# Kernel optimization log

Hardware: AMD Instinct MI355X
Metric: run time of the kernel (lower is better)

## Reference

```python
import jax, jax.numpy as jnp
import numpy as np

# Production-scale dims: batch, feature dim, number of hierarchy classes.
B, F, C = 4096, 1024, 2047
DEPTH = 11  # perfect binary tree: levels 0..10, C = 2**11 - 1, parent(i) = (i-1)//2

# Static per-level node index arrays (numpy, so the jitted code sees constants).
LEVELS = [np.arange(2 ** l - 1, 2 ** (l + 1) - 1) for l in range(DEPTH)]


def setup_inputs() -> dict:
    key = jax.random.key(0)
    k1, k2, k3 = jax.random.split(key, 3)
    x = jax.random.normal(k1, (B, F), jnp.float32)
    weight = jax.random.normal(k2, (C, F), jnp.float32) * 0.02  # nn.Linear weight (C, F)
    bias = jnp.zeros((C,), jnp.float32)
    # Original zero-inits pairs; we use small random values so the CRF is non-trivial.
    pairs = jax.random.normal(k3, (C, C, 2, 2), jnp.float32) * 0.1
    return {"x": x, "weight": weight, "bias": bias, "pairs": pairs}


def _crf_marginals(emissions, pairs):
    """Tree-CRF sum-product (forward/backward style) over a binary label tree.

    emissions: (B, C, 2) log-potentials per node per binary label.
    pairs: (C, C, 2, 2); pairs[i, j, yi, yj] is the edge potential for parent i,
    child j (only tree edges are consumed, matching TreeCRFLayer).
    Returns per-node marginal probabilities (B, C, 2).
    """
    alphas = jnp.zeros_like(emissions)
    # Upward messages: leaves -> root, one vectorized step per tree level.
    for l in range(DEPTH - 1, 0, -1):
        idx = LEVELS[l]
        par = (idx - 1) // 2
        local = emissions[:, idx] + alphas[:, idx]                    # (B, n, 2) child label
        pe = pairs[par, idx]                                          # (n, 2, 2) [y_par, y_child]
        msg = jax.nn.logsumexp(pe[None] + local[:, :, None, :], axis=3)  # (B, n, 2)
        alphas = alphas.at[:, par].add(msg)  # siblings share a parent -> scatter-add
    betas = jnp.zeros_like(emissions)
    # Downward messages: root -> leaves.
    for l in range(DEPTH - 1):
        idx = LEVELS[l]
        local = emissions[:, idx] + betas[:, idx]                     # (B, n, 2) parent label
        for ch in (2 * idx + 1, 2 * idx + 2):
            pe = pairs[idx, ch]                                       # (n, 2, 2)
            msg = jax.nn.logsumexp(local[:, :, :, None] + pe[None], axis=2)  # (B, n, 2)
            betas = betas.at[:, ch].set(msg)  # exactly one parent per node
    scores = emissions + alphas + betas
    return jax.nn.softmax(scores, axis=2)  # normalize per node over the 2 labels


def reference(x, weight, bias, pairs):
    e = x @ weight.T + bias                   # (B, C) = Linear(n_features -> n_classes)
    emissions = jnp.stack((-e, e), axis=2)    # (B, C, 2)
    return _crf_marginals(emissions, pairs)[:, :, 1]
```

## Files before the change

kernel.cpp:

```cpp
#include <hip/hip_runtime.h>
#include <math.h>

#define B_DIM 4096
#define F_DIM 1024
#define C_DIM 2047
#define C_PAD 2048
#define DEPTH 11

#define LOG2E 1.4426950408889634f

typedef __attribute__((ext_vector_type(8))) short bf16x8;
typedef __attribute__((ext_vector_type(4))) float f32x4;

#define AS1(p) ((const __attribute__((address_space(1))) void*)(p))
#define AS3(p) ((__attribute__((address_space(3))) void*)(p))

__device__ __forceinline__ unsigned short f2bf(float f) {
    unsigned int u = __float_as_uint(f);
    unsigned int r = (u + 0x7fffu + ((u >> 16) & 1u)) >> 16;
    return (unsigned short)r;
}

#define XTOT (B_DIM * F_DIM)
#define WTOT (C_PAD * F_DIM)

__global__ __launch_bounds__(256) void cvt_kernel(
    const float* __restrict__ x, const float* __restrict__ w,
    unsigned short* __restrict__ xb, unsigned short* __restrict__ wb)
{
    const int i = (blockIdx.x * 256 + threadIdx.x) * 4;
    if (i < XTOT) {
        float4 v = *(const float4*)(x + i);
        ushort4 h;
        h.x = f2bf(v.x); h.y = f2bf(v.y); h.z = f2bf(v.z); h.w = f2bf(v.w);
        *(ushort4*)(xb + i) = h;
    } else {
        const int j = i - XTOT;
        const int row = j >> 10;
        ushort4 h = {0, 0, 0, 0};
        if (row < C_DIM) {
            float4 v = *(const float4*)(w + j);
            h.x = f2bf(v.x); h.y = f2bf(v.y); h.z = f2bf(v.z); h.w = f2bf(v.w);
        }
        *(ushort4*)(wb + j) = h;
    }
}

__global__ __launch_bounds__(256) void pack_kernel(
    const float* __restrict__ pairs, float* __restrict__ pk)
{
    const int c = blockIdx.x * 256 + threadIdx.x;
    if (c >= 1 && c < C_DIM) {
        const int p = (c - 1) >> 1;
        float4 v = *(const float4*)(pairs + ((size_t)p * C_DIM + c) * 4);
        pk[c + 1]        = v.x * LOG2E;
        pk[c + 1 + 2048] = v.y * LOG2E;
        pk[c + 1 + 4096] = v.z * LOG2E;
        pk[c + 1 + 6144] = v.w * LOG2E;
    }
}

__global__ __launch_bounds__(256) void gemm_bf16_kernel(
    const unsigned short* __restrict__ xb, const unsigned short* __restrict__ wb,
    const float* __restrict__ bias, float* __restrict__ eb)
{
    __shared__ unsigned short smemA[128 * 32];
    __shared__ unsigned short smemB[128 * 32];

    const int tid  = threadIdx.x;
    const int lane = tid & 63;
    const int wave = tid >> 6;
    const int wr = wave >> 1, wc = wave & 1;

    const int lin = blockIdx.x + blockIdx.y * gridDim.x;
    const int wg  = (lin & 7) * 64 + (lin >> 3);
    const int bn = wg & 15, bm = wg >> 4;

    f32x4 acc[4][4] = {};
    const int r0 = tid >> 2,         c0 = tid & 3;
    const int r1 = (tid + 256) >> 2, c1 = tid & 3;
    const int sc0 = ((c0 ^ ((r0 >> 1) & 3)) << 3);
    const int sc1 = ((c1 ^ ((r1 >> 1) & 3)) << 3);

    const size_t arow0 = (size_t)(bm * 128 + r0) * F_DIM;
    const size_t arow1 = (size_t)(bm * 128 + r1) * F_DIM;
    const size_t brow0 = (size_t)(bn * 128 + r0) * F_DIM;
    const size_t brow1 = (size_t)(bn * 128 + r1) * F_DIM;

    unsigned short* ldsA0 = smemA + wave * 512;
    unsigned short* ldsA1 = smemA + 2048 + wave * 512;
    unsigned short* ldsB0 = smemB + wave * 512;
    unsigned short* ldsB1 = smemB + 2048 + wave * 512;

    const int fra = wr * 64 + (lane & 15);
    const int frb = wc * 64 + (lane & 15);
    const int kc  = lane >> 4;

    for (int k0 = 0; k0 < F_DIM; k0 += 32) {
        __builtin_amdgcn_global_load_lds(AS1(xb + arow0 + k0 + sc0), AS3(ldsA0), 16, 0, 0);
        __builtin_amdgcn_global_load_lds(AS1(xb + arow1 + k0 + sc1), AS3(ldsA1), 16, 0, 0);
        __builtin_amdgcn_global_load_lds(AS1(wb + brow0 + k0 + sc0), AS3(ldsB0), 16, 0, 0);
        __builtin_amdgcn_global_load_lds(AS1(wb + brow1 + k0 + sc1), AS3(ldsB1), 16, 0, 0);
        __syncthreads();

        bf16x8 af[4], bfr[4];
#pragma unroll
        for (int m = 0; m < 4; ++m) {
            const int row = fra + m * 16;
            af[m] = *(const bf16x8*)(smemA + row * 32 + ((kc ^ ((row >> 1) & 3)) << 3));
        }
#pragma unroll
        for (int n = 0; n < 4; ++n) {
            const int row = frb + n * 16;
            bfr[n] = *(const bf16x8*)(smemB + row * 32 + ((kc ^ ((row >> 1) & 3)) << 3));
        }
#pragma unroll
        for (int m = 0; m < 4; ++m)
#pragma unroll
            for (int n = 0; n < 4; ++n)
                acc[m][n] = __builtin_amdgcn_mfma_f32_16x16x32_bf16(
                    af[m], bfr[n], acc[m][n], 0, 0, 0);
        __syncthreads();
    }

    const int colbase = bn * 128 + wc * 64 + (lane & 15);
    const int rowbase = bm * 128 + wr * 64 + ((lane >> 4) << 2);
#pragma unroll
    for (int m = 0; m < 4; ++m)
#pragma unroll
        for (int n = 0; n < 4; ++n) {
            const int gc = colbase + n * 16;
            if (gc < C_DIM) {
                const float bv = bias[gc];
#pragma unroll
                for (int r = 0; r < 4; ++r)
                    eb[(size_t)(rowbase + m * 16 + r) * C_PAD + gc + 1] = acc[m][n][r] + bv;
            }
        }
}

#define BMF 64
#define BNF 64
#define BKF 16

__global__ __launch_bounds__(256) void gemm_f32_kernel(
    const float* __restrict__ x, const float* __restrict__ w,
    const float* __restrict__ bias, float* __restrict__ e)
{
    __shared__ float As[BKF][BMF];
    __shared__ float Bs[BKF][BNF];
    const int bn = blockIdx.x, bm = blockIdx.y;
    const int tid = threadIdx.x;
    const int tx = tid & 15, ty = tid >> 4;
    const int m0 = ty * 4, n0 = tx * 4;
    const int lrow = tid >> 2, lc4 = (tid & 3) * 4;
    const int gm = bm * BMF + lrow;
    const int gn = bn * BNF + lrow;
    const bool wvalid = (gn < C_DIM);
    const float* xp = x + (size_t)gm * F_DIM + lc4;
    const float* wp = wvalid ? (w + (size_t)gn * F_DIM + lc4) : w;
    float acc[4][4] = {};
    for (int k0 = 0; k0 < F_DIM; k0 += BKF) {
        float4 av = *(const float4*)(xp + k0);
        float4 bv = make_float4(0.f, 0.f, 0.f, 0.f);
        if (wvalid) bv = *(const float4*)(wp + k0);
        As[lc4 + 0][lrow] = av.x; As[lc4 + 1][lrow] = av.y;
        As[lc4 + 2][lrow] = av.z; As[lc4 + 3][lrow] = av.w;
        Bs[lc4 + 0][lrow] = bv.x; Bs[lc4 + 1][lrow] = bv.y;
        Bs[lc4 + 2][lrow] = bv.z; Bs[lc4 + 3][lrow] = bv.w;
        __syncthreads();
#pragma unroll
        for (int k = 0; k < BKF; ++k) {
            float4 a = *(const float4*)&As[k][m0];
            float4 b = *(const float4*)&Bs[k][n0];
            acc[0][0] += a.x * b.x; acc[0][1] += a.x * b.y; acc[0][2] += a.x * b.z; acc[0][3] += a.x * b.w;
            acc[1][0] += a.y * b.x; acc[1][1] += a.y * b.y; acc[1][2] += a.y * b.z; acc[1][3] += a.y * b.w;
            acc[2][0] += a.z * b.x; acc[2][1] += a.z * b.y; acc[2][2] += a.z * b.z; acc[2][3] += a.z * b.w;
            acc[3][0] += a.w * b.x; acc[3][1] += a.w * b.y; acc[3][2] += a.w * b.z; acc[3][3] += a.w * b.w;
        }
        __syncthreads();
    }
    const int gmo = bm * BMF + m0, gno = bn * BNF + n0;
#pragma unroll
    for (int i = 0; i < 4; ++i)
#pragma unroll
        for (int j = 0; j < 4; ++j) {
            int n = gno + j;
            if (n < C_DIM) e[(size_t)(gmo + i) * C_DIM + n] = acc[i][j] + bias[n];
        }
}

__device__ __forceinline__ float lse2_2(float a, float b) {
    float m = fmaxf(a, b);
    return m + __log2f(1.f + exp2f(fminf(a, b) - m));
}
__device__ __forceinline__ float sigmoid2(float d) {
    return __builtin_amdgcn_rcpf(1.f + exp2f(-d));
}

__global__ __launch_bounds__(256) void crf_wave_kernel(
    const float* __restrict__ pk,
    const float* __restrict__ eb,
    float* __restrict__ out)
{
    const int lane = threadIdx.x & 63;
    const int row  = blockIdx.x * 4 + (threadIdx.x >> 6);
    const float* ebr = eb + (size_t)row * C_PAD;
    float* orow = out + (size_t)row * C_DIM;
    const float* pkx = pk;
    const float* pky = pk + 2048;
    const float* pkz = pk + 4096;
    const float* pkw = pk + 6144;

    float el[4][4];
    float da9[4][2];
#pragma unroll
    for (int q = 0; q < 4; ++q) {
        const int bi = 1024 + 4 * lane + 256 * q;
        float4 ev = *(const float4*)(ebr + bi);
        float4 k4x = *(const float4*)(pkx + bi);
        float4 k4y = *(const float4*)(pky + bi);
        float4 k4z = *(const float4*)(pkz + bi);
        float4 k4w = *(const float4*)(pkw + bi);
        float er[4] = {ev.x * LOG2E, ev.y * LOG2E, ev.z * LOG2E, ev.w * LOG2E};
        float xr[4] = {k4x.x, k4x.y, k4x.z, k4x.w};
        float yr[4] = {k4y.x, k4y.y, k4y.z, k4y.w};
        float zr[4] = {k4z.x, k4z.y, k4z.z, k4z.w};
        float wr4[4] = {k4w.x, k4w.y, k4w.z, k4w.w};
        float dm[4];
#pragma unroll
        for (int r = 0; r < 4; ++r) {
            el[q][r] = er[r];
            dm[r] = lse2_2(zr[r] - er[r], wr4[r] + er[r])
                  - lse2_2(xr[r] - er[r], yr[r] + er[r]);
        }
        da9[q][0] = dm[0] + dm[1];
        da9[q][1] = dm[2] + dm[3];
    }

    float e9[4][2], da8[4];
#pragma unroll
    for (int q = 0; q < 4; ++q) {
        const int bi = 512 + 2 * lane + 128 * q;
        float2 ev = *(const float2*)(ebr + bi);
        float2 k2x = *(const float2*)(pkx + bi);
        float2 k2y = *(const float2*)(pky + bi);
        float2 k2z = *(const float2*)(pkz + bi);
        float2 k2w = *(const float2*)(pkw + bi);
        e9[q][0] = ev.x * LOG2E; e9[q][1] = ev.y * LOG2E;
        float dm0 = lse2_2(k2z.x - e9[q][0], k2w.x + e9[q][0] + da9[q][0])
                  - lse2_2(k2x.x - e9[q][0], k2y.x + e9[q][0] + da9[q][0]);
        float dm1 = lse2_2(k2z.y - e9[q][1], k2w.y + e9[q][1] + da9[q][1])
                  - lse2_2(k2x.y - e9[q][1], k2y.y + e9[q][1] + da9[q][1]);
        da8[q] = dm0 + dm1;
    }

    float e8[4], ps8[4];
#pragma unroll
    for (int q = 0; q < 4; ++q) {
        const int bi = 256 + lane + 64 * q;
        e8[q] = ebr[bi] * LOG2E;
        float kx = pkx[bi], ky = pky[bi], kz = pkz[bi], kw = pkw[bi];
        float dm = lse2_2(kz - e8[q], kw + e8[q] + da8[q])
                 - lse2_2(kx - e8[q], ky + e8[q] + da8[q]);
        ps8[q] = dm + __shfl_xor(dm, 1, 64);
    }
    float da7[2];
    {
        const int s = (2 * lane) & 63;
        float t00 = __shfl(ps8[0], s, 64), t01 = __shfl(ps8[1], s, 64);
        float t10 = __shfl(ps8[2], s, 64), t11 = __shfl(ps8[3], s, 64);
        da7[0] = (lane >= 32) ? t01 : t00;
        da7[1] = (lane >= 32) ? t11 : t10;
    }

    float e7[2], ps7[2];
#pragma unroll
    for (int q = 0; q < 2; ++q) {
        const int bi = 128 + lane + 64 * q;
        e7[q] = ebr[bi] * LOG2E;
        float kx = pkx[bi], ky = pky[bi], kz = pkz[bi], kw = pkw[bi];
        float dm = lse2_2(kz - e7[q], kw + e7[q] + da7[q])
                 - lse2_2(kx - e7[q], ky + e7[q] + da7[q]);
        ps7[q] = dm + __shfl_xor(dm, 1, 64);
    }
    float da6;
    {
        const int s = (2 * lane) & 63;
        float t0 = __shfl(ps7[0], s, 64), t1 = __shfl(ps7[1], s, 64);
        da6 = (lane >= 32) ? t1 : t0;
    }

    const float e6 = ebr[64 + lane] * LOG2E;
    float eup[6];
#pragma unroll
    for (int lvl = 0; lvl < 6; ++lvl)
        eup[lvl] = ebr[(1 << lvl) + lane] * LOG2E;

    float daS[6];
    {
        float da_cur = da6, e_cur = e6;
        int cb = 64;
#pragma unroll
        for (int lvl = 5; lvl >= 0; --lvl) {
            const int idx = cb + lane;
            float kx = pkx[idx], ky = pky[idx], kz = pkz[idx], kw = pkw[idx];
            float m0 = lse2_2(kx - e_cur, ky + e_cur + da_cur);
            float m1 = lse2_2(kz - e_cur, kw + e_cur + da_cur);
            float dm = m1 - m0;
            float da_new = __shfl(dm, (2 * lane) & 63, 64)
                         + __shfl(dm, (2 * lane + 1) & 63, 64);
            da_cur = da_new;
            e_cur  = eup[lvl];
            daS[lvl] = da_new;
            cb = (1 << lvl);
        }
    }

    float db_cur = 0.f;
#pragma unroll
    for (int lvl = 0; lvl < 6; ++lvl) {
        const int np = 1 << lvl;
        if (lane < np)
            orow[np - 1 + lane] = sigmoid2(2.f * eup[lvl] + daS[lvl] + db_cur);
        float pdb = __shfl(db_cur, lane >> 1, 64);
        float pe  = __shfl(eup[lvl], lane >> 1, 64);
        const int idx = 2 * np + lane;
        float kx = pkx[idx], ky = pky[idx], kz = pkz[idx], kw = pkw[idx];
        db_cur = lse2_2(-pe + ky, pe + pdb + kw) - lse2_2(-pe + kx, pe + pdb + kz);
    }
    const float db6 = db_cur;
    orow[63 + lane] = sigmoid2(2.f * e6 + da6 + db6);

    float db7[2];
#pragma unroll
    for (int q = 0; q < 2; ++q) {
        const int u = (lane >> 1) + 32 * q;
        float pe  = __shfl(e6, u, 64);
        float pdb = __shfl(db6, u, 64);
        const int bi = 128 + lane + 64 * q;
        float kx = pkx[bi], ky = pky[bi], kz = pkz[bi], kw = pkw[bi];
        db7[q] = lse2_2(-pe + ky, pe + pdb + kw) - lse2_2(-pe + kx, pe + pdb + kz);
        orow[127 + lane + 64 * q] = sigmoid2(2.f * e7[q] + da7[q] + db7[q]);
    }

    float db8[4];
#pragma unroll
    for (int q = 0; q < 4; ++q) {
        const int u  = (lane >> 1) + 32 * q;
        const int sl = u & 63;
        float pe  = __shfl(e7[q >> 1], sl, 64);
        float pdb = __shfl(db7[q >> 1], sl, 64);
        const int bi = 256 + lane + 64 * q;
        float kx = pkx[bi], ky = pky[bi], kz = pkz[bi], kw = pkw[bi];
        db8[q] = lse2_2(-pe + ky, pe + pdb + kw) - lse2_2(-pe + kx, pe + pdb + kz);
        orow[255 + lane + 64 * q] = sigmoid2(2.f * e8[q] + da8[q] + db8[q]);
    }

    float db9[4][2];
#pragma unroll
    for (int q = 0; q < 4; ++q) {
        const float lp0 = -e8[q], lp1 = e8[q] + db8[q];
        const int bi = 512 + 2 * lane + 128 * q;
        float2 k2x = *(const float2*)(pkx + bi);
        float2 k2y = *(const float2*)(pky + bi);
        float2 k2z = *(const float2*)(pkz + bi);
        float2 k2w = *(const float2*)(pkw + bi);
        db9[q][0] = lse2_2(lp0 + k2y.x, lp1 + k2w.x) - lse2_2(lp0 + k2x.x, lp1 + k2z.x);
        db9[q][1] = lse2_2(lp0 + k2y.y, lp1 + k2w.y) - lse2_2(lp0 + k2x.y, lp1 + k2z.y);
        orow[511 + 2 * lane + 128 * q]     = sigmoid2(2.f * e9[q][0] + da9[q][0] + db9[q][0]);
        orow[511 + 2 * lane + 128 * q + 1] = sigmoid2(2.f * e9[q][1] + da9[q][1] + db9[q][1]);
    }

#pragma unroll
    for (int q = 0; q < 4; ++q) {
        const int bi = 1024 + 4 * lane + 256 * q;
        float4 k4x = *(const float4*)(pkx + bi);
        float4 k4y = *(const float4*)(pky + bi);
        float4 k4z = *(const float4*)(pkz + bi);
        float4 k4w = *(const float4*)(pkw + bi);
        float xr[4] = {k4x.x, k4x.y, k4x.z, k4x.w};
        float yr[4] = {k4y.x, k4y.y, k4y.z, k4y.w};
        float zr[4] = {k4z.x, k4z.y, k4z.z, k4z.w};
        float wr4[4] = {k4w.x, k4w.y, k4w.z, k4w.w};
#pragma unroll
        for (int r = 0; r < 4; ++r) {
            const float pe = e9[q][r >> 1], pdb = db9[q][r >> 1];
            float db = lse2_2(-pe + yr[r], pe + pdb + wr4[r])
                     - lse2_2(-pe + xr[r], pe + pdb + zr[r]);
            orow[1023 + 4 * lane + 256 * q + r] = sigmoid2(2.f * el[q][r] + db);
        }
    }
}

__global__ __launch_bounds__(64) void crf_fallback_kernel(
    const float* __restrict__ pairs, float* __restrict__ eo)
{
    __shared__ float se[C_DIM];
    __shared__ float da[1023];
    __shared__ float P0[1024];
    __shared__ float P1[1024];

    const int row  = blockIdx.x;
    const int lane = threadIdx.x;
    float* erow = eo + (size_t)row * C_DIM;

    for (int c = lane; c < C_DIM; c += 64) se[c] = erow[c] * LOG2E;
    __syncthreads();

    float* cur = P0; float* nxt = P1;
    for (int l = DEPTH - 1; l >= 1; --l) {
        const int np = 1 << (l - 1);
        const int pg0 = np - 1;
        const bool leaf = (l == DEPTH - 1);
        for (int i = lane; i < np; i += 64) {
            const int p = pg0 + i;
            float a0 = 0.f, a1 = 0.f;
#pragma unroll
            for (int s = 0; s < 2; ++s) {
                const int c = 2 * p + 1 + s;
                const int jc = 2 * i + s;
                float ca0 = 0.f, ca1 = 0.f;
                if (!leaf) { ca0 = cur[jc * 2]; ca1 = cur[jc * 2 + 1]; }
                const float l0 = -se[c] + ca0;
                const float l1 =  se[c] + ca1;
                float4 pe = *(const float4*)(pairs + ((size_t)p * C_DIM + c) * 4);
                pe.x *= LOG2E; pe.y *= LOG2E; pe.z *= LOG2E; pe.w *= LOG2E;
                a0 += lse2_2(pe.x + l0, pe.y + l1);
                a1 += lse2_2(pe.z + l0, pe.w + l1);
            }
            nxt[i * 2] = a0; nxt[i * 2 + 1] = a1;
            da[p] = a1 - a0;
        }
        __syncthreads();
        float* t = cur; cur = nxt; nxt = t;
    }
    if (lane == 0) erow[0] = sigmoid2(2.f * se[0] + da[0]);

    float* bcur = P0; float* bnxt = P1;
    for (int l = 1; l <= DEPTH - 1; ++l) {
        const int nc = 1 << l;
        const int cg0 = nc - 1;
        const bool top = (l == 1), last = (l == DEPTH - 1);
        for (int j = lane; j < nc; j += 64) {
            const int c = cg0 + j;
            const int p = (c - 1) >> 1;
            const int ip = j >> 1;
            float b0 = 0.f, b1 = 0.f;
            if (!top) { b0 = bcur[ip * 2]; b1 = bcur[ip * 2 + 1]; }
            const float lp0 = -se[p] + b0;
            const float lp1 =  se[p] + b1;
            float4 pe = *(const float4*)(pairs + ((size_t)p * C_DIM + c) * 4);
            pe.x *= LOG2E; pe.y *= LOG2E; pe.z *= LOG2E; pe.w *= LOG2E;
            const float bc0 = lse2_2(lp0 + pe.x, lp1 + pe.z);
            const float bc1 = lse2_2(lp0 + pe.y, lp1 + pe.w);
            if (!last) { bnxt[j * 2] = bc0; bnxt[j * 2 + 1] = bc1; }
            float d = 2.f * se[c] + (bc1 - bc0);
            if (c < 1023) d += da[c];
            erow[c] = sigmoid2(d);
        }
        __syncthreads();
        float* t = bcur; bcur = bnxt; bnxt = t;
    }
}

extern "C" void kernel_launch(void* const* d_in, const int* in_sizes, int n_in,
                              void* d_out, int out_size, void* d_ws, size_t ws_size,
                              hipStream_t stream) {
    const float* x     = (const float*)d_in[0];
    const float* w     = (const float*)d_in[1];
    const float* bias  = (const float*)d_in[2];
    const float* pairs = (const float*)d_in[3];
    float* out = (float*)d_out;

    unsigned short* xb = (unsigned short*)d_ws;
    unsigned short* wb = xb + (size_t)XTOT;
    float* pkbuf = (float*)(wb + (size_t)WTOT);
    float* ebuf  = pkbuf + 4 * 2048;

    const size_t need = (size_t)(XTOT + WTOT) * 2 + (size_t)4 * 2048 * 4
                      + ((size_t)B_DIM * C_PAD + C_PAD) * 4;

    if (ws_size >= need) {
        cvt_kernel<<<(XTOT + WTOT) / (256 * 4), 256, 0, stream>>>(x, w, xb, wb);
        pack_kernel<<<C_PAD / 256, 256, 0, stream>>>(pairs, pkbuf);
        dim3 ggrid(C_PAD / 128, B_DIM / 128);
        gemm_bf16_kernel<<<ggrid, 256, 0, stream>>>(xb, wb, bias, ebuf);
        crf_wave_kernel<<<B_DIM / 4, 256, 0, stream>>>(pkbuf, ebuf, out);
    } else {
        dim3 ggrid((C_DIM + BNF - 1) / BNF, B_DIM / BMF);
        gemm_f32_kernel<<<ggrid, 256, 0, stream>>>(x, w, bias, out);
        crf_fallback_kernel<<<B_DIM, 64, 0, stream>>>(pairs, out);
    }
}
```

Measured before the change: 68.39 us.

## Store emissions as bf16, fuse pack into convert, process two rows per wave in CRF

The GEMM epilogue now writes emissions as bf16 instead of fp32, halving the intermediate buffer's write and read traffic. The pairs-packing kernel is merged into the input conversion kernel, removing one launch. The CRF kernel processes two batch rows per wave, so each loaded pair-potential value is reused across both rows and the grid is halved. In exchange it loses precision in the emissions and raises register pressure in the CRF kernel.

```diff
diff --git a/kernel.cpp b/kernel.cpp
--- a/kernel.cpp
+++ b/kernel.cpp
@@ -15,18 +15,23 @@
 #define AS1(p) ((const __attribute__((address_space(1))) void*)(p))
 #define AS3(p) ((__attribute__((address_space(3))) void*)(p))
 
+#define XTOT (B_DIM * F_DIM)
+#define WTOT (C_PAD * F_DIM)
+
 __device__ __forceinline__ unsigned short f2bf(float f) {
     unsigned int u = __float_as_uint(f);
     unsigned int r = (u + 0x7fffu + ((u >> 16) & 1u)) >> 16;
     return (unsigned short)r;
 }
-
-#define XTOT (B_DIM * F_DIM)
-#define WTOT (C_PAD * F_DIM)
-
-__global__ __launch_bounds__(256) void cvt_kernel(
+__device__ __forceinline__ float bf2f(unsigned short u) {
+    return __uint_as_float(((unsigned int)u) << 16);
+}
+
+__global__ __launch_bounds__(256) void cvt_pack_kernel(
     const float* __restrict__ x, const float* __restrict__ w,
-    unsigned short* __restrict__ xb, unsigned short* __restrict__ wb)
+    const float* __restrict__ pairs,
+    unsigned short* __restrict__ xb, unsigned short* __restrict__ wb,
+    float* __restrict__ pk)
 {
     const int i = (blockIdx.x * 256 + threadIdx.x) * 4;
     if (i < XTOT) {
@@ -34,7 +39,7 @@
         ushort4 h;
         h.x = f2bf(v.x); h.y = f2bf(v.y); h.z = f2bf(v.z); h.w = f2bf(v.w);
         *(ushort4*)(xb + i) = h;
-    } else {
+    } else if (i < XTOT + WTOT) {
         const int j = i - XTOT;
         const int row = j >> 10;
         ushort4 h = {0, 0, 0, 0};
@@ -43,26 +48,26 @@
             h.x = f2bf(v.x); h.y = f2bf(v.y); h.z = f2bf(v.z); h.w = f2bf(v.w);
         }
         *(ushort4*)(wb + j) = h;
-    }
-}
-
-__global__ __launch_bounds__(256) void pack_kernel(
-    const float* __restrict__ pairs, float* __restrict__ pk)
-{
-    const int c = blockIdx.x * 256 + threadIdx.x;
-    if (c >= 1 && c < C_DIM) {
-        const int p = (c - 1) >> 1;
-        float4 v = *(const float4*)(pairs + ((size_t)p * C_DIM + c) * 4);
-        pk[c + 1]        = v.x * LOG2E;
-        pk[c + 1 + 2048] = v.y * LOG2E;
-        pk[c + 1 + 4096] = v.z * LOG2E;
-        pk[c + 1 + 6144] = v.w * LOG2E;
+    } else {
+        const int c0 = i - XTOT - WTOT;
+#pragma unroll
+        for (int t = 0; t < 4; ++t) {
+            const int c = c0 + t;
+            if (c >= 1 && c < C_DIM) {
+                const int p = (c - 1) >> 1;
+                float4 v = *(const float4*)(pairs + ((size_t)p * C_DIM + c) * 4);
+                pk[c + 1]        = v.x * LOG2E;
+                pk[c + 1 + 2048] = v.y * LOG2E;
+                pk[c + 1 + 4096] = v.z * LOG2E;
+                pk[c + 1 + 6144] = v.w * LOG2E;
+            }
+        }
     }
 }
 
 __global__ __launch_bounds__(256) void gemm_bf16_kernel(
     const unsigned short* __restrict__ xb, const unsigned short* __restrict__ wb,
-    const float* __restrict__ bias, float* __restrict__ eb)
+    const float* __restrict__ bias, unsigned short* __restrict__ eb)
 {
     __shared__ unsigned short smemA[128 * 32];
     __shared__ unsigned short smemB[128 * 32];
@@ -134,7 +139,8 @@
                 const float bv = bias[gc];
 #pragma unroll
                 for (int r = 0; r < 4; ++r)
-                    eb[(size_t)(rowbase + m * 16 + r) * C_PAD + gc + 1] = acc[m][n][r] + bv;
+                    eb[(size_t)(rowbase + m * 16 + r) * C_PAD + gc + 1] =
+                        f2bf(acc[m][n][r] + bv);
             }
         }
 }
@@ -200,178 +206,21 @@
 
 __global__ __launch_bounds__(256) void crf_wave_kernel(
     const float* __restrict__ pk,
-    const float* __restrict__ eb,
+    const unsigned short* __restrict__ eb,
     float* __restrict__ out)
 {
     const int lane = threadIdx.x & 63;
-    const int row  = blockIdx.x * 4 + (threadIdx.x >> 6);
-    const float* ebr = eb + (size_t)row * C_PAD;
-    float* orow = out + (size_t)row * C_DIM;
+    const int wid  = blockIdx.x * 4 + (threadIdx.x >> 6);
+    const unsigned short* ebr[2] = {eb + (size_t)(2 * wid) * C_PAD,
+                                    eb + (size_t)(2 * wid + 1) * C_PAD};
+    float* orow[2] = {out + (size_t)(2 * wid) * C_DIM,
+                      out + (size_t)(2 * wid + 1) * C_DIM};
     const float* pkx = pk;
     const float* pky = pk + 2048;
     const float* pkz = pk + 4096;
     const float* pkw = pk + 6144;
 
-    float el[4][4];
-    float da9[4][2];
-#pragma unroll
-    for (int q = 0; q < 4; ++q) {
-        const int bi = 1024 + 4 * lane + 256 * q;
-        float4 ev = *(const float4*)(ebr + bi);
-        float4 k4x = *(const float4*)(pkx + bi);
-        float4 k4y = *(const float4*)(pky + bi);
-        float4 k4z = *(const float4*)(pkz + bi);
-        float4 k4w = *(const float4*)(pkw + bi);
-        float er[4] = {ev.x * LOG2E, ev.y * LOG2E, ev.z * LOG2E, ev.w * LOG2E};
-        float xr[4] = {k4x.x, k4x.y, k4x.z, k4x.w};
-        float yr[4] = {k4y.x, k4y.y, k4y.z, k4y.w};
-        float zr[4] = {k4z.x, k4z.y, k4z.z, k4z.w};
-        float wr4[4] = {k4w.x, k4w.y, k4w.z, k4w.w};
-        float dm[4];
-#pragma unroll
-        for (int r = 0; r < 4; ++r) {
-            el[q][r] = er[r];
-            dm[r] = lse2_2(zr[r] - er[r], wr4[r] + er[r])
-                  - lse2_2(xr[r] - er[r], yr[r] + er[r]);
-        }
-        da9[q][0] = dm[0] + dm[1];
-        da9[q][1] = dm[2] + dm[3];
-    }
-
-    float e9[4][2], da8[4];
-#pragma unroll
-    for (int q = 0; q < 4; ++q) {
-        const int bi = 512 + 2 * lane + 128 * q;
-        float2 ev = *(const float2*)(ebr + bi);
-        float2 k2x = *(const float2*)(pkx + bi);
-        float2 k2y = *(const float2*)(pky + bi);
-        float2 k2z = *(const float2*)(pkz + bi);
-        float2 k2w = *(const float2*)(pkw + bi);
-        e9[q][0] = ev.x * LOG2E; e9[q][1] = ev.y * LOG2E;
-        float dm0 = lse2_2(k2z.x - e9[q][0], k2w.x + e9[q][0] + da9[q][0])
-                  - lse2_2(k2x.x - e9[q][0], k2y.x + e9[q][0] + da9[q][0]);
-        float dm1 = lse2_2(k2z.y - e9[q][1], k2w.y + e9[q][1] + da9[q][1])
-                  - lse2_2(k2x.y - e9[q][1], k2y.y + e9[q][1] + da9[q][1]);
-        da8[q] = dm0 + dm1;
-    }
-
-    float e8[4], ps8[4];
-#pragma unroll
-    for (int q = 0; q < 4; ++q) {
-        const int bi = 256 + lane + 64 * q;
-        e8[q] = ebr[bi] * LOG2E;
-        float kx = pkx[bi], ky = pky[bi], kz = pkz[bi], kw = pkw[bi];
-        float dm = lse2_2(kz - e8[q], kw + e8[q] + da8[q])
-                 - lse2_2(kx - e8[q], ky + e8[q] + da8[q]);
-        ps8[q] = dm + __shfl_xor(dm, 1, 64);
-    }
-    float da7[2];
-    {
-        const int s = (2 * lane) & 63;
-        float t00 = __shfl(ps8[0], s, 64), t01 = __shfl(ps8[1], s, 64);
-        float t10 = __shfl(ps8[2], s, 64), t11 = __shfl(ps8[3], s, 64);
-        da7[0] = (lane >= 32) ? t01 : t00;
-        da7[1] = (lane >= 32) ? t11 : t10;
-    }
-
-    float e7[2], ps7[2];
-#pragma unroll
-    for (int q = 0; q < 2; ++q) {
-        const int bi = 128 + lane + 64 * q;
-        e7[q] = ebr[bi] * LOG2E;
-        float kx = pkx[bi], ky = pky[bi], kz = pkz[bi], kw = pkw[bi];
-        float dm = lse2_2(kz - e7[q], kw + e7[q] + da7[q])
-                 - lse2_2(kx - e7[q], ky + e7[q] + da7[q]);
-        ps7[q] = dm + __shfl_xor(dm, 1, 64);
-    }
-    float da6;
-    {
-        const int s = (2 * lane) & 63;
-        float t0 = __shfl(ps7[0], s, 64), t1 = __shfl(ps7[1], s, 64);
-        da6 = (lane >= 32) ? t1 : t0;
-    }
-
-    const float e6 = ebr[64 + lane] * LOG2E;
-    float eup[6];
-#pragma unroll
-    for (int lvl = 0; lvl < 6; ++lvl)
-        eup[lvl] = ebr[(1 << lvl) + lane] * LOG2E;
-
-    float daS[6];
-    {
-        float da_cur = da6, e_cur = e6;
-        int cb = 64;
-#pragma unroll
-        for (int lvl = 5; lvl >= 0; --lvl) {
-            const int idx = cb + lane;
-            float kx = pkx[idx], ky = pky[idx], kz = pkz[idx], kw = pkw[idx];
-            float m0 = lse2_2(kx - e_cur, ky + e_cur + da_cur);
-            float m1 = lse2_2(kz - e_cur, kw + e_cur + da_cur);
-            float dm = m1 - m0;
-            float da_new = __shfl(dm, (2 * lane) & 63, 64)
-                         + __shfl(dm, (2 * lane + 1) & 63, 64);
-            da_cur = da_new;
-            e_cur  = eup[lvl];
-            daS[lvl] = da_new;
-            cb = (1 << lvl);
-        }
-    }
-
-    float db_cur = 0.f;
-#pragma unroll
-    for (int lvl = 0; lvl < 6; ++lvl) {
-        const int np = 1 << lvl;
-        if (lane < np)
-            orow[np - 1 + lane] = sigmoid2(2.f * eup[lvl] + daS[lvl] + db_cur);
-        float pdb = __shfl(db_cur, lane >> 1, 64);
-        float pe  = __shfl(eup[lvl], lane >> 1, 64);
-        const int idx = 2 * np + lane;
-        float kx = pkx[idx], ky = pky[idx], kz = pkz[idx], kw = pkw[idx];
-        db_cur = lse2_2(-pe + ky, pe + pdb + kw) - lse2_2(-pe + kx, pe + pdb + kz);
-    }
-    const float db6 = db_cur;
-    orow[63 + lane] = sigmoid2(2.f * e6 + da6 + db6);
-
-    float db7[2];
-#pragma unroll
-    for (int q = 0; q < 2; ++q) {
-        const int u = (lane >> 1) + 32 * q;
-        float pe  = __shfl(e6, u, 64);
-        float pdb = __shfl(db6, u, 64);
-        const int bi = 128 + lane + 64 * q;
-        float kx = pkx[bi], ky = pky[bi], kz = pkz[bi], kw = pkw[bi];
-        db7[q] = lse2_2(-pe + ky, pe + pdb + kw) - lse2_2(-pe + kx, pe + pdb + kz);
-        orow[127 + lane + 64 * q] = sigmoid2(2.f * e7[q] + da7[q] + db7[q]);
-    }
-
-    float db8[4];
-#pragma unroll
-    for (int q = 0; q < 4; ++q) {
-        const int u  = (lane >> 1) + 32 * q;
-        const int sl = u & 63;
-        float pe  = __shfl(e7[q >> 1], sl, 64);
-        float pdb = __shfl(db7[q >> 1], sl, 64);
-        const int bi = 256 + lane + 64 * q;
-        float kx = pkx[bi], ky = pky[bi], kz = pkz[bi], kw = pkw[bi];
-        db8[q] = lse2_2(-pe + ky, pe + pdb + kw) - lse2_2(-pe + kx, pe + pdb + kz);
-        orow[255 + lane + 64 * q] = sigmoid2(2.f * e8[q] + da8[q] + db8[q]);
-    }
-
-    float db9[4][2];
-#pragma unroll
-    for (int q = 0; q < 4; ++q) {
-        const float lp0 = -e8[q], lp1 = e8[q] + db8[q];
-        const int bi = 512 + 2 * lane + 128 * q;
-        float2 k2x = *(const float2*)(pkx + bi);
-        float2 k2y = *(const float2*)(pky + bi);
-        float2 k2z = *(const float2*)(pkz + bi);
-        float2 k2w = *(const float2*)(pkw + bi);
-        db9[q][0] = lse2_2(lp0 + k2y.x, lp1 + k2w.x) - lse2_2(lp0 + k2x.x, lp1 + k2z.x);
-        db9[q][1] = lse2_2(lp0 + k2y.y, lp1 + k2w.y) - lse2_2(lp0 + k2x.y, lp1 + k2z.y);
-        orow[511 + 2 * lane + 128 * q]     = sigmoid2(2.f * e9[q][0] + da9[q][0] + db9[q][0]);
-        orow[511 + 2 * lane + 128 * q + 1] = sigmoid2(2.f * e9[q][1] + da9[q][1] + db9[q][1]);
-    }
-
+    float el[2][4][4], da9[2][4][2];
 #pragma unroll
     for (int q = 0; q < 4; ++q) {
         const int bi = 1024 + 4 * lane + 256 * q;
@@ -384,11 +233,226 @@
         float zr[4] = {k4z.x, k4z.y, k4z.z, k4z.w};
         float wr4[4] = {k4w.x, k4w.y, k4w.z, k4w.w};
 #pragma unroll
-        for (int r = 0; r < 4; ++r) {
-            const float pe = e9[q][r >> 1], pdb = db9[q][r >> 1];
-            float db = lse2_2(-pe + yr[r], pe + pdb + wr4[r])
-                     - lse2_2(-pe + xr[r], pe + pdb + zr[r]);
-            orow[1023 + 4 * lane + 256 * q + r] = sigmoid2(2.f * el[q][r] + db);
+        for (int rr = 0; rr < 2; ++rr) {
+            ushort4 ev = *(const ushort4*)(ebr[rr] + bi);
+            float er[4] = {bf2f(ev.x) * LOG2E, bf2f(ev.y) * LOG2E,
+                           bf2f(ev.z) * LOG2E, bf2f(ev.w) * LOG2E};
+            float dm[4];
+#pragma unroll
+            for (int r = 0; r < 4; ++r) {
+                el[rr][q][r] = er[r];
+                dm[r] = lse2_2(zr[r] - er[r], wr4[r] + er[r])
+                      - lse2_2(xr[r] - er[r], yr[r] + er[r]);
+            }
+            da9[rr][q][0] = dm[0] + dm[1];
+            da9[rr][q][1] = dm[2] + dm[3];
+        }
+    }
+
+    float e9[2][4][2], da8[2][4];
+#pragma unroll
+    for (int q = 0; q < 4; ++q) {
+        const int bi = 512 + 2 * lane + 128 * q;
+        float2 k2x = *(const float2*)(pkx + bi);
+        float2 k2y = *(const float2*)(pky + bi);
+        float2 k2z = *(const float2*)(pkz + bi);
+        float2 k2w = *(const float2*)(pkw + bi);
+#pragma unroll
+        for (int rr = 0; rr < 2; ++rr) {
+            ushort2 ev = *(const ushort2*)(ebr[rr] + bi);
+            float e0 = bf2f(ev.x) * LOG2E, e1 = bf2f(ev.y) * LOG2E;
+            e9[rr][q][0] = e0; e9[rr][q][1] = e1;
+            float dm0 = lse2_2(k2z.x - e0, k2w.x + e0 + da9[rr][q][0])
+                      - lse2_2(k2x.x - e0, k2y.x + e0 + da9[rr][q][0]);
+            float dm1 = lse2_2(k2z.y - e1, k2w.y + e1 + da9[rr][q][1])
+                      - lse2_2(k2x.y - e1, k2y.y + e1 + da9[rr][q][1]);
+            da8[rr][q] = dm0 + dm1;
+        }
+    }
+
+    float e8[2][4], ps8[2][4];
+#pragma unroll
+    for (int q = 0; q < 4; ++q) {
+        const int bi = 256 + lane + 64 * q;
+        float kx = pkx[bi], ky = pky[bi], kz = pkz[bi], kw = pkw[bi];
+#pragma unroll
+        for (int rr = 0; rr < 2; ++rr) {
+            float e = bf2f(ebr[rr][bi]) * LOG2E;
+            e8[rr][q] = e;
+            float dm = lse2_2(kz - e, kw + e + da8[rr][q])
+                     - lse2_2(kx - e, ky + e + da8[rr][q]);
+            ps8[rr][q] = dm + __shfl_xor(dm, 1, 64);
+        }
+    }
+    float da7[2][2];
+    {
+        const int s = (2 * lane) & 63;
+#pragma unroll
+        for (int rr = 0; rr < 2; ++rr) {
+            float t00 = __shfl(ps8[rr][0], s, 64), t01 = __shfl(ps8[rr][1], s, 64);
+            float t10 = __shfl(ps8[rr][2], s, 64), t11 = __shfl(ps8[rr][3], s, 64);
+            da7[rr][0] = (lane >= 32) ? t01 : t00;
+            da7[rr][1] = (lane >= 32) ? t11 : t10;
+        }
+    }
+
+    float e7[2][2], ps7[2][2];
+#pragma unroll
+    for (int q = 0; q < 2; ++q) {
+        const int bi = 128 + lane + 64 * q;
+        float kx = pkx[bi], ky = pky[bi], kz = pkz[bi], kw = pkw[bi];
+#pragma unroll
+        for (int rr = 0; rr < 2; ++rr) {
+            float e = bf2f(ebr[rr][bi]) * LOG2E;
+            e7[rr][q] = e;
+            float dm = lse2_2(kz - e, kw + e + da7[rr][q])
+                     - lse2_2(kx - e, ky + e + da7[rr][q]);
+            ps7[rr][q] = dm + __shfl_xor(dm, 1, 64);
+        }
+    }
+    float da6[2];
+    {
+        const int s = (2 * lane) & 63;
+#pragma unroll
+        for (int rr = 0; rr < 2; ++rr) {
+            float t0 = __shfl(ps7[rr][0], s, 64), t1 = __shfl(ps7[rr][1], s, 64);
+            da6[rr] = (lane >= 32) ? t1 : t0;
+        }
+    }
+
+    float e6[2], eup[2][6];
+#pragma unroll
+    for (int rr = 0; rr < 2; ++rr) {
+        e6[rr] = bf2f(ebr[rr][64 + lane]) * LOG2E;
+#pragma unroll
+        for (int lvl = 0; lvl < 6; ++lvl)
+            eup[rr][lvl] = bf2f(ebr[rr][(1 << lvl) + lane]) * LOG2E;
+    }
+
+    float daS[2][6];
+    {
+        float da_cur[2] = {da6[0], da6[1]};
+        float e_cur[2]  = {e6[0], e6[1]};
+        int cb = 64;
+#pragma unroll
+        for (int lvl = 5; lvl >= 0; --lvl) {
+            const int idx = cb + lane;
+            float kx = pkx[idx], ky = pky[idx], kz = pkz[idx], kw = pkw[idx];
+#pragma unroll
+            for (int rr = 0; rr < 2; ++rr) {
+                float m0 = lse2_2(kx - e_cur[rr], ky + e_cur[rr] + da_cur[rr]);
+                float m1 = lse2_2(kz - e_cur[rr], kw + e_cur[rr] + da_cur[rr]);
+                float dm = m1 - m0;
+                float da_new = __shfl(dm, (2 * lane) & 63, 64)
+                             + __shfl(dm, (2 * lane + 1) & 63, 64);
+                da_cur[rr] = da_new;
+                e_cur[rr]  = eup[rr][lvl];
+                daS[rr][lvl] = da_new;
+            }
+            cb = (1 << lvl);
+        }
+    }
+
+    float db_cur[2] = {0.f, 0.f};
+#pragma unroll
+    for (int lvl = 0; lvl < 6; ++lvl) {
+        const int np = 1 << lvl;
+        const int idx = 2 * np + lane;
+        float kx = pkx[idx], ky = pky[idx], kz = pkz[idx], kw = pkw[idx];
+#pragma unroll
+        for (int rr = 0; rr < 2; ++rr) {
+            if (lane < np)
+                orow[rr][np - 1 + lane] =
+                    sigmoid2(2.f * eup[rr][lvl] + daS[rr][lvl] + db_cur[rr]);
+            float pdb = __shfl(db_cur[rr], lane >> 1, 64);
+            float pe  = __shfl(eup[rr][lvl], lane >> 1, 64);
+            db_cur[rr] = lse2_2(-pe + ky, pe + pdb + kw)
+                       - lse2_2(-pe + kx, pe + pdb + kz);
+        }
+    }
+    float db6[2] = {db_cur[0], db_cur[1]};
+#pragma unroll
+    for (int rr = 0; rr < 2; ++rr)
+        orow[rr][63 + lane] = sigmoid2(2.f * e6[rr] + da6[rr] + db6[rr]);
+
+    float db7[2][2];
+#pragma unroll
+    for (int q = 0; q < 2; ++q) {
+        const int u = (lane >> 1) + 32 * q;
+        const int bi = 128 + lane + 64 * q;
+        float kx = pkx[bi], ky = pky[bi], kz = pkz[bi], kw = pkw[bi];
+#pragma unroll
+        for (int rr = 0; rr < 2; ++rr) {
+            float pe  = __shfl(e6[rr], u, 64);
+            float pdb = __shfl(db6[rr], u, 64);
+            db7[rr][q] = lse2_2(-pe + ky, pe + pdb + kw)
+                       - lse2_2(-pe + kx, pe + pdb + kz);
+            orow[rr][127 + lane + 64 * q] =
+                sigmoid2(2.f * e7[rr][q] + da7[rr][q] + db7[rr][q]);
+        }
+    }
+
+    float db8[2][4];
+#pragma unroll
+    for (int q = 0; q < 4; ++q) {
+        const int u  = (lane >> 1) + 32 * q;
+        const int sl = u & 63;
+        const int bi = 256 + lane + 64 * q;
+        float kx = pkx[bi], ky = pky[bi], kz = pkz[bi], kw = pkw[bi];
+#pragma unroll
+        for (int rr = 0; rr < 2; ++rr) {
+            float pe  = __shfl(e7[rr][q >> 1], sl, 64);
+            float pdb = __shfl(db7[rr][q >> 1], sl, 64);
+            db8[rr][q] = lse2_2(-pe + ky, pe + pdb + kw)
+                       - lse2_2(-pe + kx, pe + pdb + kz);
+            orow[rr][255 + lane + 64 * q] =
+                sigmoid2(2.f * e8[rr][q] + da8[rr][q] + db8[rr][q]);
+        }
+    }
+
+    float db9[2][4][2];
+#pragma unroll
+    for (int q = 0; q < 4; ++q) {
+        const int bi = 512 + 2 * lane + 128 * q;
+        float2 k2x = *(const float2*)(pkx + bi);
+        float2 k2y = *(const float2*)(pky + bi);
+        float2 k2z = *(const float2*)(pkz + bi);
+        float2 k2w = *(const float2*)(pkw + bi);
+#pragma unroll
+        for (int rr = 0; rr < 2; ++rr) {
+            const float lp0 = -e8[rr][q], lp1 = e8[rr][q] + db8[rr][q];
+            db9[rr][q][0] = lse2_2(lp0 + k2y.x, lp1 + k2w.x)
+                          - lse2_2(lp0 + k2x.x, lp1 + k2z.x);
+            db9[rr][q][1] = lse2_2(lp0 + k2y.y, lp1 + k2w.y)
+                          - lse2_2(lp0 + k2x.y, lp1 + k2z.y);
+            orow[rr][511 + 2 * lane + 128 * q] =
+                sigmoid2(2.f * e9[rr][q][0] + da9[rr][q][0] + db9[rr][q][0]);
+            orow[rr][511 + 2 * lane + 128 * q + 1] =
+                sigmoid2(2.f * e9[rr][q][1] + da9[rr][q][1] + db9[rr][q][1]);
+        }
+    }
+
+#pragma unroll
+    for (int q = 0; q < 4; ++q) {
+        const int bi = 1024 + 4 * lane + 256 * q;
+        float4 k4x = *(const float4*)(pkx + bi);
+        float4 k4y = *(const float4*)(pky + bi);
+        float4 k4z = *(const float4*)(pkz + bi);
+        float4 k4w = *(const float4*)(pkw + bi);
+        float xr[4] = {k4x.x, k4x.y, k4x.z, k4x.w};
+        float yr[4] = {k4y.x, k4y.y, k4y.z, k4y.w};
+        float zr[4] = {k4z.x, k4z.y, k4z.z, k4z.w};
+        float wr4[4] = {k4w.x, k4w.y, k4w.z, k4w.w};
+#pragma unroll
+        for (int rr = 0; rr < 2; ++rr) {
+#pragma unroll
+            for (int r = 0; r < 4; ++r) {
+                const float pe = e9[rr][q][r >> 1], pdb = db9[rr][q][r >> 1];
+                float db = lse2_2(-pe + yr[r], pe + pdb + wr4[r])
+                         - lse2_2(-pe + xr[r], pe + pdb + zr[r]);
+                orow[rr][1023 + 4 * lane + 256 * q + r] =
+                    sigmoid2(2.f * el[rr][q][r] + db);
+            }
         }
     }
 }
@@ -476,17 +540,17 @@
     unsigned short* xb = (unsigned short*)d_ws;
     unsigned short* wb = xb + (size_t)XTOT;
     float* pkbuf = (float*)(wb + (size_t)WTOT);
-    float* ebuf  = pkbuf + 4 * 2048;
+    unsigned short* ebuf = (unsigned short*)(pkbuf + 4 * 2048);
 
     const size_t need = (size_t)(XTOT + WTOT) * 2 + (size_t)4 * 2048 * 4
-                      + ((size_t)B_DIM * C_PAD + C_PAD) * 4;
+                      + ((size_t)B_DIM * C_PAD + C_PAD) * 2;
 
     if (ws_size >= need) {
-        cvt_kernel<<<(XTOT + WTOT) / (256 * 4), 256, 0, stream>>>(x, w, xb, wb);
-        pack_kernel<<<C_PAD / 256, 256, 0, stream>>>(pairs, pkbuf);
+        cvt_pack_kernel<<<(XTOT + WTOT + 2048) / (256 * 4), 256, 0, stream>>>(
+            x, w, pairs, xb, wb, pkbuf);
         dim3 ggrid(C_PAD / 128, B_DIM / 128);
         gemm_bf16_kernel<<<ggrid, 256, 0, stream>>>(xb, wb, bias, ebuf);
-        crf_wave_kernel<<<B_DIM / 4, 256, 0, stream>>>(pkbuf, ebuf, out);
+        crf_wave_kernel<<<B_DIM / 8, 256, 0, stream>>>(pkbuf, ebuf, out);
     } else {
         dim3 ggrid((C_DIM + BNF - 1) / BNF, B_DIM / BMF);
         gemm_f32_kernel<<<ggrid, 256, 0, stream>>>(x, w, bias, out);
```

New measurement: 65.37 us. 1.05x faster.
